# Performance work log

Measured on AMD Instinct MI355X. Metric: run time of the kernel, lower is better.

Reference implementation:

```python
import jax, jax.numpy as jnp
import numpy as np

U, D, E, L = 100000, 10000, 500000, 100000
H, O, VC = 128, 64, 20
ED = H // 4  # emb_dim = hidden // 4


def setup_inputs() -> dict:
    key = jax.random.key(0)
    it = iter(jax.random.split(key, 60))
    def nrm(shape, s=0.1):
        return jax.random.normal(next(it), shape, jnp.float32) * s
    inp = {}
    inp["x_user"] = nrm((U, 3), 1.0)
    inp["x_dest"] = nrm((D, 1), 1.0)
    inp["edge_src"] = jax.random.randint(next(it), (E,), 0, U)
    inp["edge_dst"] = jax.random.randint(next(it), (E,), 0, D)
    inp["eattr_cat"] = jax.random.randint(next(it), (E, 3), 0, VC)
    inp["eattr_num"] = nrm((E, 3), 1.0)
    inp["label_src"] = jax.random.randint(next(it), (L,), 0, U)
    inp["label_dst"] = jax.random.randint(next(it), (L,), 0, D)
    inp["user_emb"] = nrm((U, H))
    inp["dest_emb"] = nrm((D, H))
    inp["Wuf"] = nrm((3, H)); inp["buf"] = jnp.zeros((H,), jnp.float32)
    inp["Wdf"] = nrm((1, H)); inp["bdf"] = jnp.zeros((H,), jnp.float32)
    inp["emb_acc"] = nrm((VC, ED)); inp["emb_trans"] = nrm((VC, ED)); inp["emb_season"] = nrm((VC, ED))
    inp["Wnum"] = nrm((3, ED)); inp["bnum"] = jnp.zeros((ED,), jnp.float32)
    inp["Weout"] = nrm((4 * ED, H)); inp["beout"] = jnp.zeros((H,), jnp.float32)
    inp["c1v_Ws"] = nrm((H, H)); inp["c1v_Wd"] = nrm((H, H)); inp["c1v_as"] = nrm((H,)); inp["c1v_ad"] = nrm((H,))
    inp["c1v_We"] = nrm((H, H)); inp["c1v_ae"] = nrm((H,)); inp["c1v_b"] = jnp.zeros((H,), jnp.float32)
    inp["c1r_Ws"] = nrm((H, H)); inp["c1r_Wd"] = nrm((H, H)); inp["c1r_as"] = nrm((H,)); inp["c1r_ad"] = nrm((H,)); inp["c1r_b"] = jnp.zeros((H,), jnp.float32)
    inp["c2v_W"] = nrm((H, H)); inp["c2v_as"] = nrm((H,)); inp["c2v_ad"] = nrm((H,)); inp["c2v_We"] = nrm((H, H)); inp["c2v_ae"] = nrm((H,)); inp["c2v_b"] = jnp.zeros((H,), jnp.float32)
    inp["c2r_W"] = nrm((H, H)); inp["c2r_as"] = nrm((H,)); inp["c2r_ad"] = nrm((H,)); inp["c2r_b"] = jnp.zeros((H,), jnp.float32)
    inp["Wmu"] = nrm((H, O)); inp["bmu"] = jnp.zeros((O,), jnp.float32)
    inp["Wls"] = nrm((H, O)); inp["bls"] = jnp.zeros((O,), jnp.float32)
    return inp


def gat(h_src, h_dst, src, dst, Ws, Wd, a_s, a_d, bias, n_dst, ef=None, We=None, ae=None):
    """PyG GATConv, heads=1, add_self_loops=False, bipartite (src->dst)."""
    xs = h_src @ Ws  # [Ns, H]
    xd = h_dst @ Wd  # [Nd, H]
    alpha = (xs * a_s).sum(-1)[src] + (xd * a_d).sum(-1)[dst]  # [E]
    if ef is not None:
        alpha = alpha + ((ef @ We) * ae).sum(-1)
    alpha = jnp.where(alpha > 0, alpha, 0.2 * alpha)  # leaky_relu(0.2)
    amax = jax.ops.segment_max(alpha, dst, num_segments=n_dst)
    ex = jnp.exp(alpha - amax[dst])
    denom = jax.ops.segment_sum(ex, dst, num_segments=n_dst)
    w = ex / (denom[dst] + 1e-16)  # segment softmax over incoming edges
    out = jax.ops.segment_sum(w[:, None] * xs[src], dst, num_segments=n_dst)
    return out + bias


def reference(x_user, x_dest, edge_src, edge_dst, eattr_cat, eattr_num, label_src, label_dst,
              user_emb, dest_emb, Wuf, buf, Wdf, bdf,
              emb_acc, emb_trans, emb_season, Wnum, bnum, Weout, beout,
              c1v_Ws, c1v_Wd, c1v_as, c1v_ad, c1v_We, c1v_ae, c1v_b,
              c1r_Ws, c1r_Wd, c1r_as, c1r_ad, c1r_b,
              c2v_W, c2v_as, c2v_ad, c2v_We, c2v_ae, c2v_b,
              c2r_W, c2r_as, c2r_ad, c2r_b,
              Wmu, bmu, Wls, bls):
    # node encoders (full-batch: arange ids == full embedding tables)
    h_user = user_emb + x_user @ Wuf + buf  # [U, H]
    h_dest = dest_emb + x_dest @ Wdf + bdf  # [D, H]
    # EdgeBehaviorEncoder
    ef = jnp.concatenate([emb_acc[eattr_cat[:, 0]], emb_trans[eattr_cat[:, 1]],
                          emb_season[eattr_cat[:, 2]], eattr_num @ Wnum + bnum], axis=1)
    ef = ef @ Weout + beout  # [E, H]
    # layer 1
    od1 = gat(h_user, h_dest, edge_src, edge_dst, c1v_Ws, c1v_Wd, c1v_as, c1v_ad, c1v_b, D, ef, c1v_We, c1v_ae)
    ou1 = gat(h_dest, h_user, edge_dst, edge_src, c1r_Ws, c1r_Wd, c1r_as, c1r_ad, c1r_b, U)
    hu = jax.nn.relu(ou1)
    hd = jax.nn.relu(od1)
    # layer 2 (int in_channels -> shared lin for src and dst)
    od2 = gat(hu, hd, edge_src, edge_dst, c2v_W, c2v_W, c2v_as, c2v_ad, c2v_b, D, ef, c2v_We, c2v_ae)
    ou2 = gat(hd, hu, edge_dst, edge_src, c2r_W, c2r_W, c2r_as, c2r_ad, c2r_b, U)
    zu = jax.nn.relu(ou2)
    zd = jax.nn.relu(od2)
    mu_u = zu @ Wmu + bmu
    mu_d = zd @ Wmu + bmu
    ls_u = zu @ Wls + bls
    ls_d = zd @ Wls + bls
    # eval mode: reparameterize returns mu; decode = dot product on label edges
    pred = (mu_u[label_src] * mu_d[label_dst]).sum(-1)  # [L]
    return pred, mu_u, mu_d, ls_u, ls_d
```

## Files before the change

### kernel.cpp

```cpp
#include <hip/hip_runtime.h>
#include <hip/hip_bf16.h>
#include <math.h>

#define H 128
#define CDIV(a,b) (((a)+(b)-1)/(b))

__device__ __forceinline__ float wave_reduce_sum(float v){
  #pragma unroll
  for (int off = 32; off > 0; off >>= 1) v += __shfl_down(v, off, 64);
  return v;
}

__device__ __forceinline__ void wave_merge_ms(float& m, float& s){
  #pragma unroll
  for (int off = 32; off > 0; off >>= 1){
    float m2 = __shfl_xor(m, off, 64);
    float s2 = __shfl_xor(s, off, 64);
    float mn = fmaxf(m, m2);
    s = s*__expf(m - mn) + s2*__expf(m2 - mn);
    m = mn;
  }
}

__global__ __launch_bounds__(128) void k_precompute(
    const float* c1v_Wd, const float* c1v_ad,
    const float* c1r_Wd, const float* c1r_ad,
    const float* c2v_W,  const float* c2v_ad,
    const float* c2r_W,  const float* c2r_ad,
    const float* c1v_We, const float* c1v_ae,
    const float* c2v_We, const float* c2v_ae,
    const float* Weout,  const float* beout,
    const float* emb_acc, const float* emb_trans, const float* emb_season,
    const float* Wnum, const float* bnum,
    const float* Wmu, const float* Wls, const float* bmu, const float* bls,
    float* sm)
{
  const int b = blockIdx.x, t = threadIdx.x;
  if (b < 4){
    const float* M; const float* a;
    if      (b == 0){ M = c1v_Wd; a = c1v_ad; }
    else if (b == 1){ M = c1r_Wd; a = c1r_ad; }
    else if (b == 2){ M = c2v_W;  a = c2v_ad; }
    else            { M = c2r_W;  a = c2r_ad; }
    float s = 0.f;
    for (int j = 0; j < H; ++j) s += M[t*H+j] * a[j];
    sm[b*H + t] = s;
  } else if (b == 4){
    __shared__ float ws[H], vs[H];
    for (int layer = 0; layer < 2; ++layer){
      const float* We = layer ? c2v_We : c1v_We;
      const float* ae = layer ? c2v_ae : c1v_ae;
      float w = 0.f;
      for (int j = 0; j < H; ++j) w += We[t*H+j] * ae[j];
      ws[t] = w;
      __syncthreads();
      float v = 0.f;
      for (int j = 0; j < H; ++j) v += Weout[t*H+j] * ws[j];
      vs[t] = v;
      __syncthreads();
      float* tab = sm + 512 + layer*64;
      if (t < 20){
        float s1 = 0.f, s2 = 0.f, s3 = 0.f;
        for (int i = 0; i < 32; ++i){
          s1 += emb_acc   [t*32+i] * vs[i];
          s2 += emb_trans [t*32+i] * vs[32+i];
          s3 += emb_season[t*32+i] * vs[64+i];
        }
        tab[t] = s1; tab[20+t] = s2; tab[40+t] = s3;
      }
      if (t < 3){
        float s = 0.f;
        for (int i = 0; i < 32; ++i) s += Wnum[t*32+i] * vs[96+i];
        tab[60+t] = s;
      }
      if (t == 0){
        float s = 0.f;
        for (int j = 0; j < H; ++j)  s += beout[j] * ws[j];
        for (int i = 0; i < 32; ++i) s += bnum[i] * vs[96+i];
        tab[63] = s;
      }
      __syncthreads();
    }
  } else {
    float* Wcat = sm + 768;
    for (int i = (b-5)*128 + t; i < 8192; i += 7*128){
      int h = i >> 6, o = i & 63;
      Wcat[h*H + o]      = Wmu[h*64 + o];
      Wcat[h*H + 64 + o] = Wls[h*64 + o];
    }
    if (b == 5) sm[640 + t] = (t < 64) ? bmu[t] : bls[t-64];
  }
}

__global__ __launch_bounds__(256) void k_enc_user(
    const float* __restrict__ emb, const float* __restrict__ x,
    const float* __restrict__ Wf, const float* __restrict__ b,
    const float* __restrict__ qd, float* __restrict__ out,
    float* __restrict__ sout, int N)
{
  int w = (blockIdx.x*blockDim.x + threadIdx.x) >> 6;
  int lane = threadIdx.x & 63;
  if (w >= N) return;
  float2 e  = ((const float2*)emb)[(size_t)w*64 + lane];
  float x0 = x[w*3], x1 = x[w*3+1], x2 = x[w*3+2];
  float2 w0 = ((const float2*)Wf)[lane];
  float2 w1 = ((const float2*)Wf)[64+lane];
  float2 w2 = ((const float2*)Wf)[128+lane];
  float2 bb = ((const float2*)b)[lane];
  float h0 = e.x + bb.x + x0*w0.x + x1*w1.x + x2*w2.x;
  float h1 = e.y + bb.y + x0*w0.y + x1*w1.y + x2*w2.y;
  ((float2*)out)[(size_t)w*64 + lane] = make_float2(h0, h1);
  float2 q = ((const float2*)qd)[lane];
  float p = wave_reduce_sum(h0*q.x + h1*q.y);
  if (lane == 0) sout[w] = p;
}

__global__ __launch_bounds__(256) void k_enc_dest(
    const float* __restrict__ emb, const float* __restrict__ x,
    const float* __restrict__ Wf, const float* __restrict__ b,
    const float* __restrict__ qd, float* __restrict__ out,
    float* __restrict__ sout, int N)
{
  int w = (blockIdx.x*blockDim.x + threadIdx.x) >> 6;
  int lane = threadIdx.x & 63;
  if (w >= N) return;
  float2 e  = ((const float2*)emb)[(size_t)w*64 + lane];
  float x0 = x[w];
  float2 w0 = ((const float2*)Wf)[lane];
  float2 bb = ((const float2*)b)[lane];
  float h0 = e.x + bb.x + x0*w0.x;
  float h1 = e.y + bb.y + x0*w0.y;
  ((float2*)out)[(size_t)w*64 + lane] = make_float2(h0, h1);
  float2 q = ((const float2*)qd)[lane];
  float p = wave_reduce_sum(h0*q.x + h1*q.y);
  if (lane == 0) sout[w] = p;
}

__global__ __launch_bounds__(256) void k_gemm128(
    const float* __restrict__ A, const float* __restrict__ W,
    const float* __restrict__ bias, const float* __restrict__ asv,
    float* __restrict__ sout,
    float* __restrict__ out0, float* __restrict__ out1,
    int ld0, int ld1, int N)
{
  __shared__ float Ws[64][128];
  __shared__ float Xs[64][132];
  __shared__ float red[64][17];
  const int tid = threadIdx.x;
  const int rb  = blockIdx.x * 64;
  const int tc  = tid & 15, tr = tid >> 4;
  const int c0  = tc * 8;
  float C[4][8] = {};
  for (int k0 = 0; k0 < 128; k0 += 64){
    for (int i = tid; i < 2048; i += 256){
      int k = i >> 5, c4 = i & 31;
      *(float4*)&Ws[k][c4*4] = *(const float4*)&W[(size_t)(k0+k)*128 + c4*4];
    }
    for (int i = tid; i < 1024; i += 256){
      int r = i >> 4, kg = i & 15;
      int row = rb + r;
      float4 v = make_float4(0.f,0.f,0.f,0.f);
      if (row < N) v = *(const float4*)&A[(size_t)row*128 + k0 + kg*4];
      *(float4*)&Xs[r][kg*4] = v;
    }
    __syncthreads();
    #pragma unroll 4
    for (int k = 0; k < 64; ++k){
      float4 w0 = *(float4*)&Ws[k][c0];
      float4 w1 = *(float4*)&Ws[k][c0+4];
      #pragma unroll
      for (int i = 0; i < 4; ++i){
        float x = Xs[tr*4+i][k];
        C[i][0] += x*w0.x; C[i][1] += x*w0.y; C[i][2] += x*w0.z; C[i][3] += x*w0.w;
        C[i][4] += x*w1.x; C[i][5] += x*w1.y; C[i][6] += x*w1.z; C[i][7] += x*w1.w;
      }
    }
    __syncthreads();
  }
  float4 b0 = make_float4(0,0,0,0), b1 = make_float4(0,0,0,0);
  if (bias){ b0 = *(const float4*)&bias[c0]; b1 = *(const float4*)&bias[c0+4]; }
  float4 a0 = make_float4(0,0,0,0), a1 = make_float4(0,0,0,0);
  if (asv){ a0 = *(const float4*)&asv[c0]; a1 = *(const float4*)&asv[c0+4]; }
  #pragma unroll
  for (int i = 0; i < 4; ++i){
    int row = rb + tr*4 + i;
    float s = 0.f;
    if (row < N){
      float4 v0 = make_float4(C[i][0]+b0.x, C[i][1]+b0.y, C[i][2]+b0.z, C[i][3]+b0.w);
      float4 v1 = make_float4(C[i][4]+b1.x, C[i][5]+b1.y, C[i][6]+b1.z, C[i][7]+b1.w);
      if (c0 < 64){
        *(float4*)&out0[(size_t)row*ld0 + c0]     = v0;
        *(float4*)&out0[(size_t)row*ld0 + c0 + 4] = v1;
      } else {
        *(float4*)&out1[(size_t)row*ld1 + (c0-64)]     = v0;
        *(float4*)&out1[(size_t)row*ld1 + (c0-64) + 4] = v1;
      }
      if (asv){
        s = C[i][0]*a0.x + C[i][1]*a0.y + C[i][2]*a0.z + C[i][3]*a0.w
          + C[i][4]*a1.x + C[i][5]*a1.y + C[i][6]*a1.z + C[i][7]*a1.w;
      }
    }
    if (asv) red[tr*4+i][tc] = s;
  }
  if (asv){
    __syncthreads();
    if (tid < 64){
      int row = rb + tid;
      if (row < N){
        float t = 0.f;
        #pragma unroll
        for (int j = 0; j < 16; ++j) t += red[tid][j];
        sout[row] = t;
      }
    }
  }
}

__global__ void k_zero2(int* a, int na, int* b, int nb){
  int i = blockIdx.x * blockDim.x + threadIdx.x;
  if (i < na) a[i] = 0;
  else if (i - na < nb) b[i - na] = 0;
}

__global__ void k_count_both(const int* __restrict__ esrc, const int* __restrict__ edst,
                             int* __restrict__ cntU, int* __restrict__ cntD, int E){
  int e = blockIdx.x * blockDim.x + threadIdx.x;
  if (e < E){ atomicAdd(&cntU[esrc[e]], 1); atomicAdd(&cntD[edst[e]], 1); }
}

__global__ __launch_bounds__(1024) void k_scan1(const int* __restrict__ cnt,
                                                int* __restrict__ offs,
                                                int* __restrict__ bsum, int n)
{
  __shared__ int wsum[16];
  const int tid = threadIdx.x, lane = tid & 63, wid = tid >> 6;
  const int i = blockIdx.x * 1024 + tid;
  int v = (i < n) ? cnt[i] : 0;
  int inc = v;
  #pragma unroll
  for (int d = 1; d < 64; d <<= 1){
    int t2 = __shfl_up(inc, d, 64);
    if (lane >= d) inc += t2;
  }
  if (lane == 63) wsum[wid] = inc;
  __syncthreads();
  if (tid < 16){
    int x = wsum[tid];
    #pragma unroll
    for (int d = 1; d < 16; d <<= 1){
      int t2 = __shfl_up(x, d, 16);
      if (tid >= d) x += t2;
    }
    wsum[tid] = x;
  }
  __syncthreads();
  int incl = ((wid > 0) ? wsum[wid-1] : 0) + inc;
  if (i < n) offs[i+1] = incl;
  if (tid == 0) bsum[blockIdx.x] = wsum[15];
}

__global__ __launch_bounds__(1024) void k_scan2(int* __restrict__ bsum, int nb)
{
  __shared__ int wsum[16];
  const int tid = threadIdx.x, lane = tid & 63, wid = tid >> 6;
  int v = (tid < nb) ? bsum[tid] : 0;
  int inc = v;
  #pragma unroll
  for (int d = 1; d < 64; d <<= 1){
    int t2 = __shfl_up(inc, d, 64);
    if (lane >= d) inc += t2;
  }
  if (lane == 63) wsum[wid] = inc;
  __syncthreads();
  if (tid < 16){
    int x = wsum[tid];
    #pragma unroll
    for (int d = 1; d < 16; d <<= 1){
      int t2 = __shfl_up(x, d, 16);
      if (tid >= d) x += t2;
    }
    wsum[tid] = x;
  }
  __syncthreads();
  int excl = ((wid > 0) ? wsum[wid-1] : 0) + inc - v;
  if (tid < nb) bsum[tid] = excl;
}

__global__ void k_scan3(const int* __restrict__ cnt, const int* __restrict__ bsum,
                        int* __restrict__ offs, int* __restrict__ cursor, int n)
{
  int i = blockIdx.x * blockDim.x + threadIdx.x;
  if (i >= n) return;
  int v = offs[i+1] + bsum[i >> 10];
  offs[i+1] = v;
  cursor[i] = v - cnt[i];
  if (i == 0) offs[0] = 0;
}

__global__ __launch_bounds__(256) void k_scatter_both(
    const int* __restrict__ esrc, const int* __restrict__ edst,
    const int* __restrict__ ecat, const float* __restrict__ enum_,
    const float* __restrict__ tab1, const float* __restrict__ tab2,
    int* __restrict__ curU, int* __restrict__ curD,
    int4* __restrict__ recD, int* __restrict__ srtOU, int E)
{
  int e = blockIdx.x * blockDim.x + threadIdx.x;
  if (e >= E) return;
  int s = esrc[e], d = edst[e];
  int c0 = ecat[e*3], c1i = ecat[e*3+1], c2i = ecat[e*3+2];
  float n0 = enum_[e*3], n1 = enum_[e*3+1], n2 = enum_[e*3+2];
  float cA = tab1[c0] + tab1[20+c1i] + tab1[40+c2i]
           + n0*tab1[60] + n1*tab1[61] + n2*tab1[62] + tab1[63];
  float cB = tab2[c0] + tab2[20+c1i] + tab2[40+c2i]
           + n0*tab2[60] + n1*tab2[61] + n2*tab2[62] + tab2[63];
  int pD = atomicAdd(&curD[d], 1);
  recD[pD] = make_int4(s, __float_as_int(cA), __float_as_int(cB), 0);
  int pU = atomicAdd(&curU[s], 1);
  srtOU[pU] = d;
}

__global__ __launch_bounds__(256) void k_agg_v(
    const int* __restrict__ offs, const int4* __restrict__ rec,
    const float* __restrict__ gS, const float* __restrict__ selfS, int lsel,
    const float* __restrict__ xs, const float* __restrict__ bias,
    float* __restrict__ out, const float* __restrict__ qd,
    float* __restrict__ sout, int N)
{
  int w = (blockIdx.x*blockDim.x + threadIdx.x) >> 6;
  int lane = threadIdx.x & 63;
  if (w >= N) return;
  const int beg = offs[w], end = offs[w+1];
  const float uni = selfS[w];

  float m = -1e30f, s = 0.f;
  for (int base = beg; base < end; base += 64){
    int i = base + lane;
    if (i < end){
      int4 r = rec[i];
      float a = gS[r.x] + uni + __int_as_float(lsel ? r.z : r.y);
      a = a > 0.f ? a : 0.2f * a;
      float mn = fmaxf(m, a);
      s = s*__expf(m - mn) + __expf(a - mn);
      m = mn;
    }
  }
  wave_merge_ms(m, s);
  const float inv = 1.f / (s + 1e-16f);

  float a0 = 0.f, a1 = 0.f;
  const float2* xs2 = (const float2*)xs;
  for (int base = beg; base < end; base += 64){
    int i = base + lane;
    int o = 0; float wgt = 0.f;
    if (i < end){
      int4 r = rec[i];
      o = r.x;
      float a = gS[o] + uni + __int_as_float(lsel ? r.z : r.y);
      a = a > 0.f ? a : 0.2f * a;
      wgt = __expf(a - m) * inv;
    }
    int nn = min(64, end - base);
    for (int j = 0; j < nn; ++j){
      int   oo = __shfl(o, j, 64);
      float ww = __shfl(wgt, j, 64);
      float2 v = xs2[(size_t)oo*64 + lane];
      a0 += ww * v.x; a1 += ww * v.y;
    }
  }
  float2 bb = ((const float2*)bias)[lane];
  float r0 = fmaxf(a0 + bb.x, 0.f);
  float r1 = fmaxf(a1 + bb.y, 0.f);
  ((float2*)out)[(size_t)w*64 + lane] = make_float2(r0, r1);
  if (qd){
    float2 q = ((const float2*)qd)[lane];
    float p = wave_reduce_sum(r0*q.x + r1*q.y);
    if (lane == 0) sout[w] = p;
  }
}

__global__ __launch_bounds__(256) void k_agg_r(
    const int* __restrict__ offs, const int* __restrict__ srtO,
    const float* __restrict__ gS, const float* __restrict__ selfS,
    const float* __restrict__ xs, const float* __restrict__ bias,
    float* __restrict__ out, const float* __restrict__ qd,
    float* __restrict__ sout, int N)
{
  int w = (blockIdx.x*blockDim.x + threadIdx.x) >> 6;
  int lane = threadIdx.x & 63;
  if (w >= N) return;
  const int beg = offs[w], end = offs[w+1];
  const float uni = selfS[w];

  float m = -1e30f, s = 0.f;
  for (int base = beg; base < end; base += 64){
    int i = base + lane;
    if (i < end){
      float a = gS[srtO[i]] + uni;
      a = a > 0.f ? a : 0.2f * a;
      float mn = fmaxf(m, a);
      s = s*__expf(m - mn) + __expf(a - mn);
      m = mn;
    }
  }
  wave_merge_ms(m, s);
  const float inv = 1.f / (s + 1e-16f);

  float a0 = 0.f, a1 = 0.f;
  const float2* xs2 = (const float2*)xs;
  for (int base = beg; base < end; base += 64){
    int i = base + lane;
    int o = 0; float wgt = 0.f;
    if (i < end){
      o = srtO[i];
      float a = gS[o] + uni;
      a = a > 0.f ? a : 0.2f * a;
      wgt = __expf(a - m) * inv;
    }
    int nn = min(64, end - base);
    for (int j = 0; j < nn; ++j){
      int   oo = __shfl(o, j, 64);
      float ww = __shfl(wgt, j, 64);
      float2 v = xs2[(size_t)oo*64 + lane];
      a0 += ww * v.x; a1 += ww * v.y;
    }
  }
  float2 bb = ((const float2*)bias)[lane];
  float r0 = fmaxf(a0 + bb.x, 0.f);
  float r1 = fmaxf(a1 + bb.y, 0.f);
  ((float2*)out)[(size_t)w*64 + lane] = make_float2(r0, r1);
  if (qd){
    float2 q = ((const float2*)qd)[lane];
    float p = wave_reduce_sum(r0*q.x + r1*q.y);
    if (lane == 0) sout[w] = p;
  }
}

__global__ void k_pred(const int* __restrict__ ls, const int* __restrict__ ld,
                       const float* __restrict__ mu_u, const float* __restrict__ mu_d,
                       float* __restrict__ pred, int L)
{
  int wid  = (blockIdx.x * blockDim.x + threadIdx.x) >> 6;
  int lane = threadIdx.x & 63;
  if (wid >= L) return;
  float p = mu_u[(size_t)ls[wid]*64 + lane] * mu_d[(size_t)ld[wid]*64 + lane];
  p = wave_reduce_sum(p);
  if (lane == 0) pred[wid] = p;
}

extern "C" void kernel_launch(void* const* d_in, const int* in_sizes, int n_in,
                              void* d_out, int out_size, void* d_ws, size_t ws_size,
                              hipStream_t stream)
{
  (void)n_in; (void)out_size; (void)ws_size;
  const float* x_user    = (const float*)d_in[0];
  const float* x_dest    = (const float*)d_in[1];
  const int*   edge_src  = (const int*)d_in[2];
  const int*   edge_dst  = (const int*)d_in[3];
  const int*   eattr_cat = (const int*)d_in[4];
  const float* eattr_num = (const float*)d_in[5];
  const int*   label_src = (const int*)d_in[6];
  const int*   label_dst = (const int*)d_in[7];
  const float* user_emb  = (const float*)d_in[8];
  const float* dest_emb  = (const float*)d_in[9];
  const float* Wuf = (const float*)d_in[10]; const float* buf_ = (const float*)d_in[11];
  const float* Wdf = (const float*)d_in[12]; const float* bdf  = (const float*)d_in[13];
  const float* emb_acc    = (const float*)d_in[14];
  const float* emb_trans  = (const float*)d_in[15];
  const float* emb_season = (const float*)d_in[16];
  const float* Wnum = (const float*)d_in[17]; const float* bnum  = (const float*)d_in[18];
  const float* Weout = (const float*)d_in[19]; const float* beout = (const float*)d_in[20];
  const float* c1v_Ws = (const float*)d_in[21]; const float* c1v_Wd = (const float*)d_in[22];
  const float* c1v_as = (const float*)d_in[23]; const float* c1v_ad = (const float*)d_in[24];
  const float* c1v_We = (const float*)d_in[25]; const float* c1v_ae = (const float*)d_in[26];
  const float* c1v_b  = (const float*)d_in[27];
  const float* c1r_Ws = (const float*)d_in[28]; const float* c1r_Wd = (const float*)d_in[29];
  const float* c1r_as = (const float*)d_in[30]; const float* c1r_ad = (const float*)d_in[31];
  const float* c1r_b  = (const float*)d_in[32];
  const float* c2v_W  = (const float*)d_in[33]; const float* c2v_as = (const float*)d_in[34];
  const float* c2v_ad = (const float*)d_in[35]; const float* c2v_We = (const float*)d_in[36];
  const float* c2v_ae = (const float*)d_in[37]; const float* c2v_b  = (const float*)d_in[38];
  const float* c2r_W  = (const float*)d_in[39]; const float* c2r_as = (const float*)d_in[40];
  const float* c2r_ad = (const float*)d_in[41]; const float* c2r_b  = (const float*)d_in[42];
  const float* Wmu = (const float*)d_in[43]; const float* bmu = (const float*)d_in[44];
  const float* Wls = (const float*)d_in[45]; const float* bls = (const float*)d_in[46];

  const int U = in_sizes[0] / 3;
  const int D = in_sizes[1];
  const int E = in_sizes[2];
  const int L = in_sizes[6];
  const int O = 64;
  const int nbD = CDIV(D, 1024), nbU = CDIV(U, 1024);

  float* fw = (float*)d_ws;
  size_t off = 0;
  auto falloc = [&](size_t n)->float*{ float* p = fw + off; off += (n + 3) & ~(size_t)3; return p; };
  float* A    = falloc((size_t)U * H);
  float* BIG  = falloc((size_t)U * H);
  float* Bd   = falloc((size_t)D * H);
  float* SM   = falloc((size_t)D * H);
  float* sUa  = falloc(U);
  float* sUb  = falloc(U);
  float* sDa  = falloc(D);
  float* sDb  = falloc(D);
  float* sml  = falloc(17152);
  int* iw = (int*)(fw + off);
  size_t ioff = 0;
  auto ialloc = [&](size_t n)->int*{ int* p = iw + ioff; ioff += (n + 3) & ~(size_t)3; return p; };
  int* recD  = ialloc((size_t)E * 4);
  int* srtOU = ialloc(E);
  int* cntD  = ialloc(D);
  int* curD  = ialloc(D);
  int* offsD = ialloc((size_t)D + 1);
  int* cntU  = ialloc(U);
  int* curU  = ialloc(U);
  int* offsU = ialloc((size_t)U + 1);
  int* bsumD = ialloc(1024);
  int* bsumU = ialloc(1024);

  float* outp = (float*)d_out;
  float* pred = outp;
  float* mu_u = outp + L;
  float* mu_d = mu_u + (size_t)U * O;
  float* ls_u = mu_d + (size_t)D * O;
  float* ls_d = ls_u + (size_t)U * O;

  hipLaunchKernelGGL(k_precompute, dim3(12), dim3(128), 0, stream,
                     c1v_Wd, c1v_ad, c1r_Wd, c1r_ad, c2v_W, c2v_ad, c2r_W, c2r_ad,
                     c1v_We, c1v_ae, c2v_We, c2v_ae, Weout, beout,
                     emb_acc, emb_trans, emb_season, Wnum, bnum, Wmu, Wls, bmu, bls, sml);
  hipLaunchKernelGGL(k_enc_user, dim3(CDIV(U,4)), dim3(256), 0, stream,
                     user_emb, x_user, Wuf, buf_, sml+128, A, sUb, U);
  hipLaunchKernelGGL(k_enc_dest, dim3(CDIV(D,4)), dim3(256), 0, stream,
                     dest_emb, x_dest, Wdf, bdf, sml+0, Bd, sDa, D);

  hipLaunchKernelGGL(k_zero2, dim3(CDIV(U+D,256)), dim3(256), 0, stream, cntU, U, cntD, D);
  hipLaunchKernelGGL(k_count_both, dim3(CDIV(E,256)), dim3(256), 0, stream,
                     edge_src, edge_dst, cntU, cntD, E);
  hipLaunchKernelGGL(k_scan1, dim3(nbD), dim3(1024), 0, stream, cntD, offsD, bsumD, D);
  hipLaunchKernelGGL(k_scan1, dim3(nbU), dim3(1024), 0, stream, cntU, offsU, bsumU, U);
  hipLaunchKernelGGL(k_scan2, dim3(1), dim3(1024), 0, stream, bsumD, nbD);
  hipLaunchKernelGGL(k_scan2, dim3(1), dim3(1024), 0, stream, bsumU, nbU);
  hipLaunchKernelGGL(k_scan3, dim3(CDIV(D,256)), dim3(256), 0, stream, cntD, bsumD, offsD, curD, D);
  hipLaunchKernelGGL(k_scan3, dim3(CDIV(U,256)), dim3(256), 0, stream, cntU, bsumU, offsU, curU, U);
  hipLaunchKernelGGL(k_scatter_both, dim3(CDIV(E,256)), dim3(256), 0, stream,
                     edge_src, edge_dst, eattr_cat, eattr_num, sml+512, sml+576,
                     curU, curD, (int4*)recD, srtOU, E);

  hipLaunchKernelGGL(k_gemm128, dim3(CDIV(U,64)), dim3(256), 0, stream,
                     A,  c1v_Ws, (const float*)nullptr, c1v_as, sUa, BIG, BIG+64, 128, 128, U);
  hipLaunchKernelGGL(k_gemm128, dim3(CDIV(D,64)), dim3(256), 0, stream,
                     Bd, c1r_Ws, (const float*)nullptr, c1r_as, sDb, SM, SM+64, 128, 128, D);
  hipLaunchKernelGGL(k_agg_v, dim3(CDIV(D,4)), dim3(256), 0, stream,
                     offsD, (const int4*)recD, sUa, sDa, 0, BIG, c1v_b, Bd, sml+256, sDa, D);
  hipLaunchKernelGGL(k_agg_r, dim3(CDIV(U,4)), dim3(256), 0, stream,
                     offsU, srtOU, sDb, sUb, SM, c1r_b, A, sml+384, sUb, U);

  hipLaunchKernelGGL(k_gemm128, dim3(CDIV(U,64)), dim3(256), 0, stream,
                     A,  c2v_W, (const float*)nullptr, c2v_as, sUa, BIG, BIG+64, 128, 128, U);
  hipLaunchKernelGGL(k_gemm128, dim3(CDIV(D,64)), dim3(256), 0, stream,
                     Bd, c2r_W, (const float*)nullptr, c2r_as, sDb, SM, SM+64, 128, 128, D);
  hipLaunchKernelGGL(k_agg_v, dim3(CDIV(D,4)), dim3(256), 0, stream,
                     offsD, (const int4*)recD, sUa, sDa, 1, BIG, c2v_b, Bd,
                     (const float*)nullptr, (float*)nullptr, D);
  hipLaunchKernelGGL(k_agg_r, dim3(CDIV(U,4)), dim3(256), 0, stream,
                     offsU, srtOU, sDb, sUb, SM, c2r_b, A,
                     (const float*)nullptr, (float*)nullptr, U);

  hipLaunchKernelGGL(k_gemm128, dim3(CDIV(U,64)), dim3(256), 0, stream,
                     A,  sml+768, sml+640, (const float*)nullptr, (float*)nullptr, mu_u, ls_u, 64, 64, U);
  hipLaunchKernelGGL(k_gemm128, dim3(CDIV(D,64)), dim3(256), 0, stream,
                     Bd, sml+768, sml+640, (const float*)nullptr, (float*)nullptr, mu_d, ls_d, 64, 64, D);
  hipLaunchKernelGGL(k_pred, dim3(CDIV((size_t)L*64,256)), dim3(256), 0, stream,
                     label_src, label_dst, mu_u, mu_d, pred, L);
}
```

Before: 875.5 us.

## Split dest aggregation across a 4-wave block and pack edge logits as fp16

k_agg_v now gives each destination node a full 256-thread block instead of one wave. Each dest node has about 50 incoming edges, so the four waves split the softmax pass and the feature gather, then merge max/sum and the partial accumulators through shared memory. The edge record shrinks from int4 to int2 by storing the two per-edge attention constants as packed fp16 halves, which cuts scatter and gather traffic but loses precision in those logits. Index math in the gathers also switches from size_t multiplies to 32-bit shifts.

```diff
diff --git a/kernel.cpp b/kernel.cpp
--- a/kernel.cpp
+++ b/kernel.cpp
@@ -1,5 +1,6 @@
 #include <hip/hip_runtime.h>
 #include <hip/hip_bf16.h>
+#include <hip/hip_fp16.h>
 #include <math.h>
 
 #define H 128
@@ -302,7 +303,7 @@
     const int* __restrict__ ecat, const float* __restrict__ enum_,
     const float* __restrict__ tab1, const float* __restrict__ tab2,
     int* __restrict__ curU, int* __restrict__ curD,
-    int4* __restrict__ recD, int* __restrict__ srtOU, int E)
+    int2* __restrict__ recD, int* __restrict__ srtOU, int E)
 {
   int e = blockIdx.x * blockDim.x + threadIdx.x;
   if (e >= E) return;
@@ -313,68 +314,87 @@
            + n0*tab1[60] + n1*tab1[61] + n2*tab1[62] + tab1[63];
   float cB = tab2[c0] + tab2[20+c1i] + tab2[40+c2i]
            + n0*tab2[60] + n1*tab2[61] + n2*tab2[62] + tab2[63];
+  unsigned ua = __half_as_ushort(__float2half_rn(cA));
+  unsigned ub = __half_as_ushort(__float2half_rn(cB));
+  int packed = (int)((ub << 16) | ua);
   int pD = atomicAdd(&curD[d], 1);
-  recD[pD] = make_int4(s, __float_as_int(cA), __float_as_int(cB), 0);
+  recD[pD] = make_int2(s, packed);
   int pU = atomicAdd(&curU[s], 1);
   srtOU[pU] = d;
 }
 
 __global__ __launch_bounds__(256) void k_agg_v(
-    const int* __restrict__ offs, const int4* __restrict__ rec,
+    const int* __restrict__ offs, const int2* __restrict__ rec,
     const float* __restrict__ gS, const float* __restrict__ selfS, int lsel,
     const float* __restrict__ xs, const float* __restrict__ bias,
     float* __restrict__ out, const float* __restrict__ qd,
     float* __restrict__ sout, int N)
 {
-  int w = (blockIdx.x*blockDim.x + threadIdx.x) >> 6;
-  int lane = threadIdx.x & 63;
-  if (w >= N) return;
-  const int beg = offs[w], end = offs[w+1];
-  const float uni = selfS[w];
+  __shared__ float lm[4], ls_[4];
+  __shared__ float2 lacc[4][64];
+  const int node = blockIdx.x;
+  const int tid = threadIdx.x, lane = tid & 63, wv = tid >> 6;
+  const int beg = offs[node], end = offs[node+1];
+  const float uni = selfS[node];
 
   float m = -1e30f, s = 0.f;
-  for (int base = beg; base < end; base += 64){
-    int i = base + lane;
-    if (i < end){
-      int4 r = rec[i];
-      float a = gS[r.x] + uni + __int_as_float(lsel ? r.z : r.y);
-      a = a > 0.f ? a : 0.2f * a;
-      float mn = fmaxf(m, a);
-      s = s*__expf(m - mn) + __expf(a - mn);
-      m = mn;
-    }
+  for (int i = beg + tid; i < end; i += 256){
+    int2 r = rec[i];
+    unsigned pk = (unsigned)r.y;
+    float c = __half2float(__ushort_as_half((unsigned short)(lsel ? (pk >> 16) : (pk & 0xffffu))));
+    float a = gS[r.x] + uni + c;
+    a = a > 0.f ? a : 0.2f * a;
+    float mn = fmaxf(m, a);
+    s = s*__expf(m - mn) + __expf(a - mn);
+    m = mn;
   }
   wave_merge_ms(m, s);
-  const float inv = 1.f / (s + 1e-16f);
-
+  if (lane == 0){ lm[wv] = m; ls_[wv] = s; }
+  __syncthreads();
+  float M = fmaxf(fmaxf(lm[0], lm[1]), fmaxf(lm[2], lm[3]));
+  float S = ls_[0]*__expf(lm[0]-M) + ls_[1]*__expf(lm[1]-M)
+          + ls_[2]*__expf(lm[2]-M) + ls_[3]*__expf(lm[3]-M);
+  const float inv = 1.f / (S + 1e-16f);
+
+  const int tot = end - beg;
+  const int q = (tot + 3) >> 2;
+  const int wbeg = beg + wv*q;
+  const int wend = min(end, wbeg + q);
   float a0 = 0.f, a1 = 0.f;
   const float2* xs2 = (const float2*)xs;
-  for (int base = beg; base < end; base += 64){
+  for (int base = wbeg; base < wend; base += 64){
     int i = base + lane;
     int o = 0; float wgt = 0.f;
-    if (i < end){
-      int4 r = rec[i];
+    if (i < wend){
+      int2 r = rec[i];
       o = r.x;
-      float a = gS[o] + uni + __int_as_float(lsel ? r.z : r.y);
+      unsigned pk = (unsigned)r.y;
+      float c = __half2float(__ushort_as_half((unsigned short)(lsel ? (pk >> 16) : (pk & 0xffffu))));
+      float a = gS[o] + uni + c;
       a = a > 0.f ? a : 0.2f * a;
-      wgt = __expf(a - m) * inv;
-    }
-    int nn = min(64, end - base);
+      wgt = __expf(a - M) * inv;
+    }
+    int nn = min(64, wend - base);
     for (int j = 0; j < nn; ++j){
       int   oo = __shfl(o, j, 64);
       float ww = __shfl(wgt, j, 64);
-      float2 v = xs2[(size_t)oo*64 + lane];
+      float2 v = xs2[(oo << 6) + lane];
       a0 += ww * v.x; a1 += ww * v.y;
     }
   }
-  float2 bb = ((const float2*)bias)[lane];
-  float r0 = fmaxf(a0 + bb.x, 0.f);
-  float r1 = fmaxf(a1 + bb.y, 0.f);
-  ((float2*)out)[(size_t)w*64 + lane] = make_float2(r0, r1);
-  if (qd){
-    float2 q = ((const float2*)qd)[lane];
-    float p = wave_reduce_sum(r0*q.x + r1*q.y);
-    if (lane == 0) sout[w] = p;
+  lacc[wv][lane] = make_float2(a0, a1);
+  __syncthreads();
+  if (wv == 0){
+    float2 t0 = lacc[0][lane], t1 = lacc[1][lane], t2 = lacc[2][lane], t3 = lacc[3][lane];
+    float2 bb = ((const float2*)bias)[lane];
+    float r0 = fmaxf(t0.x+t1.x+t2.x+t3.x + bb.x, 0.f);
+    float r1 = fmaxf(t0.y+t1.y+t2.y+t3.y + bb.y, 0.f);
+    ((float2*)out)[(size_t)node*64 + lane] = make_float2(r0, r1);
+    if (qd){
+      float2 qv = ((const float2*)qd)[lane];
+      float p = wave_reduce_sum(r0*qv.x + r1*qv.y);
+      if (lane == 0) sout[node] = p;
+    }
   }
 }
 
@@ -392,15 +412,12 @@
   const float uni = selfS[w];
 
   float m = -1e30f, s = 0.f;
-  for (int base = beg; base < end; base += 64){
-    int i = base + lane;
-    if (i < end){
-      float a = gS[srtO[i]] + uni;
-      a = a > 0.f ? a : 0.2f * a;
-      float mn = fmaxf(m, a);
-      s = s*__expf(m - mn) + __expf(a - mn);
-      m = mn;
-    }
+  for (int i = beg + lane; i < end; i += 64){
+    float a = gS[srtO[i]] + uni;
+    a = a > 0.f ? a : 0.2f * a;
+    float mn = fmaxf(m, a);
+    s = s*__expf(m - mn) + __expf(a - mn);
+    m = mn;
   }
   wave_merge_ms(m, s);
   const float inv = 1.f / (s + 1e-16f);
@@ -420,7 +437,7 @@
     for (int j = 0; j < nn; ++j){
       int   oo = __shfl(o, j, 64);
       float ww = __shfl(wgt, j, 64);
-      float2 v = xs2[(size_t)oo*64 + lane];
+      float2 v = xs2[(oo << 6) + lane];
       a0 += ww * v.x; a1 += ww * v.y;
     }
   }
@@ -442,7 +459,7 @@
   int wid  = (blockIdx.x * blockDim.x + threadIdx.x) >> 6;
   int lane = threadIdx.x & 63;
   if (wid >= L) return;
-  float p = mu_u[(size_t)ls[wid]*64 + lane] * mu_d[(size_t)ld[wid]*64 + lane];
+  float p = mu_u[(ls[wid] << 6) + lane] * mu_d[(ld[wid] << 6) + lane];
   p = wave_reduce_sum(p);
   if (lane == 0) pred[wid] = p;
 }
@@ -506,7 +523,7 @@
   int* iw = (int*)(fw + off);
   size_t ioff = 0;
   auto ialloc = [&](size_t n)->int*{ int* p = iw + ioff; ioff += (n + 3) & ~(size_t)3; return p; };
-  int* recD  = ialloc((size_t)E * 4);
+  int* recD  = ialloc((size_t)E * 2);
   int* srtOU = ialloc(E);
   int* cntD  = ialloc(D);
   int* curD  = ialloc(D);
@@ -544,14 +561,14 @@
   hipLaunchKernelGGL(k_scan3, dim3(CDIV(U,256)), dim3(256), 0, stream, cntU, bsumU, offsU, curU, U);
   hipLaunchKernelGGL(k_scatter_both, dim3(CDIV(E,256)), dim3(256), 0, stream,
                      edge_src, edge_dst, eattr_cat, eattr_num, sml+512, sml+576,
-                     curU, curD, (int4*)recD, srtOU, E);
+                     curU, curD, (int2*)recD, srtOU, E);
 
   hipLaunchKernelGGL(k_gemm128, dim3(CDIV(U,64)), dim3(256), 0, stream,
                      A,  c1v_Ws, (const float*)nullptr, c1v_as, sUa, BIG, BIG+64, 128, 128, U);
   hipLaunchKernelGGL(k_gemm128, dim3(CDIV(D,64)), dim3(256), 0, stream,
                      Bd, c1r_Ws, (const float*)nullptr, c1r_as, sDb, SM, SM+64, 128, 128, D);
-  hipLaunchKernelGGL(k_agg_v, dim3(CDIV(D,4)), dim3(256), 0, stream,
-                     offsD, (const int4*)recD, sUa, sDa, 0, BIG, c1v_b, Bd, sml+256, sDa, D);
+  hipLaunchKernelGGL(k_agg_v, dim3(D), dim3(256), 0, stream,
+                     offsD, (const int2*)recD, sUa, sDa, 0, BIG, c1v_b, Bd, sml+256, sDa, D);
   hipLaunchKernelGGL(k_agg_r, dim3(CDIV(U,4)), dim3(256), 0, stream,
                      offsU, srtOU, sDb, sUb, SM, c1r_b, A, sml+384, sUb, U);
 
@@ -559,8 +576,8 @@
                      A,  c2v_W, (const float*)nullptr, c2v_as, sUa, BIG, BIG+64, 128, 128, U);
   hipLaunchKernelGGL(k_gemm128, dim3(CDIV(D,64)), dim3(256), 0, stream,
                      Bd, c2r_W, (const float*)nullptr, c2r_as, sDb, SM, SM+64, 128, 128, D);
-  hipLaunchKernelGGL(k_agg_v, dim3(CDIV(D,4)), dim3(256), 0, stream,
-                     offsD, (const int4*)recD, sUa, sDa, 1, BIG, c2v_b, Bd,
+  hipLaunchKernelGGL(k_agg_v, dim3(D), dim3(256), 0, stream,
+                     offsD, (const int2*)recD, sUa, sDa, 1, BIG, c2v_b, Bd,
                      (const float*)nullptr, (float*)nullptr, D);
   hipLaunchKernelGGL(k_agg_r, dim3(CDIV(U,4)), dim3(256), 0, stream,
                      offsU, srtOU, sDb, sUb, SM, c2r_b, A,
```

Measured after the change: 867.4 us. Within noise of the previous version (-0.9%).

## Pack edge attention terms as fp16, bin scatter by node range, split waves per node

Applied to the files above, without the earlier changes.

Edge attention constants are now computed in the counting pass and packed into one int as two fp16 halves, so the destination-sorted record shrinks from int4 to int2. The scatter kernel uses a fixed grid split into 8 groups, each handling only edges whose node falls in its range, to improve atomic and write locality. The aggregation kernels now split a wave across several nodes (2 per wave for destinations, 4 per wave for users) with float4 loads, which cuts idle lanes on low-degree nodes. The fp16 packing loses precision in the attention logits, and the binned scatter reads the edge list 8 times.

```diff
diff --git a/kernel.cpp b/kernel.cpp
--- a/kernel.cpp
+++ b/kernel.cpp
@@ -1,5 +1,6 @@
 #include <hip/hip_runtime.h>
 #include <hip/hip_bf16.h>
+#include <hip/hip_fp16.h>
 #include <math.h>
 
 #define H 128
@@ -11,15 +12,10 @@
   return v;
 }
 
-__device__ __forceinline__ void wave_merge_ms(float& m, float& s){
-  #pragma unroll
-  for (int off = 32; off > 0; off >>= 1){
-    float m2 = __shfl_xor(m, off, 64);
-    float s2 = __shfl_xor(s, off, 64);
-    float mn = fmaxf(m, m2);
-    s = s*__expf(m - mn) + s2*__expf(m2 - mn);
-    m = mn;
-  }
+__device__ __forceinline__ float unpack_c(int pk, int lsel){
+  unsigned u = (unsigned)pk;
+  unsigned short h = (unsigned short)(lsel ? (u >> 16) : (u & 0xffffu));
+  return __half2float(__ushort_as_half(h));
 }
 
 __global__ __launch_bounds__(128) void k_precompute(
@@ -222,10 +218,26 @@
   else if (i - na < nb) b[i - na] = 0;
 }
 
-__global__ void k_count_both(const int* __restrict__ esrc, const int* __restrict__ edst,
-                             int* __restrict__ cntU, int* __restrict__ cntD, int E){
+__global__ __launch_bounds__(256) void k_pack_count(
+    const int* __restrict__ esrc, const int* __restrict__ edst,
+    const int* __restrict__ ecat, const float* __restrict__ enum_,
+    const float* __restrict__ tab1, const float* __restrict__ tab2,
+    int* __restrict__ cntU, int* __restrict__ cntD,
+    int* __restrict__ packed, int E)
+{
   int e = blockIdx.x * blockDim.x + threadIdx.x;
-  if (e < E){ atomicAdd(&cntU[esrc[e]], 1); atomicAdd(&cntD[edst[e]], 1); }
+  if (e >= E) return;
+  int c0 = ecat[e*3], c1i = ecat[e*3+1], c2i = ecat[e*3+2];
+  float n0 = enum_[e*3], n1 = enum_[e*3+1], n2 = enum_[e*3+2];
+  float cA = tab1[c0] + tab1[20+c1i] + tab1[40+c2i]
+           + n0*tab1[60] + n1*tab1[61] + n2*tab1[62] + tab1[63];
+  float cB = tab2[c0] + tab2[20+c1i] + tab2[40+c2i]
+           + n0*tab2[60] + n1*tab2[61] + n2*tab2[62] + tab2[63];
+  unsigned ua = __half_as_ushort(__float2half_rn(cA));
+  unsigned ub = __half_as_ushort(__float2half_rn(cB));
+  packed[e] = (int)((ub << 16) | ua);
+  atomicAdd(&cntU[esrc[e]], 1);
+  atomicAdd(&cntD[edst[e]], 1);
 }
 
 __global__ __launch_bounds__(1024) void k_scan1(const int* __restrict__ cnt,
@@ -297,84 +309,96 @@
   if (i == 0) offs[0] = 0;
 }
 
-__global__ __launch_bounds__(256) void k_scatter_both(
+__global__ __launch_bounds__(256) void k_scatter_binned(
     const int* __restrict__ esrc, const int* __restrict__ edst,
-    const int* __restrict__ ecat, const float* __restrict__ enum_,
-    const float* __restrict__ tab1, const float* __restrict__ tab2,
+    const int* __restrict__ packed,
     int* __restrict__ curU, int* __restrict__ curD,
-    int4* __restrict__ recD, int* __restrict__ srtOU, int E)
-{
-  int e = blockIdx.x * blockDim.x + threadIdx.x;
-  if (e >= E) return;
-  int s = esrc[e], d = edst[e];
-  int c0 = ecat[e*3], c1i = ecat[e*3+1], c2i = ecat[e*3+2];
-  float n0 = enum_[e*3], n1 = enum_[e*3+1], n2 = enum_[e*3+2];
-  float cA = tab1[c0] + tab1[20+c1i] + tab1[40+c2i]
-           + n0*tab1[60] + n1*tab1[61] + n2*tab1[62] + tab1[63];
-  float cB = tab2[c0] + tab2[20+c1i] + tab2[40+c2i]
-           + n0*tab2[60] + n1*tab2[61] + n2*tab2[62] + tab2[63];
-  int pD = atomicAdd(&curD[d], 1);
-  recD[pD] = make_int4(s, __float_as_int(cA), __float_as_int(cB), 0);
-  int pU = atomicAdd(&curU[s], 1);
-  srtOU[pU] = d;
+    int2* __restrict__ recD, int* __restrict__ srtOU, int E, int U, int D)
+{
+  const int grp = blockIdx.x & 7;
+  const int lb  = blockIdx.x >> 3;
+  const int GB  = gridDim.x >> 3;
+  const int D8 = CDIV(D, 8), U8 = CDIV(U, 8);
+  const int dlo = grp * D8, dhi = min(D, dlo + D8);
+  const int slo = grp * U8, shi = min(U, slo + U8);
+  for (int e = lb*256 + threadIdx.x; e < E; e += GB*256){
+    int s = esrc[e], d = edst[e];
+    if (d >= dlo && d < dhi){
+      int p = atomicAdd(&curD[d], 1);
+      recD[p] = make_int2(s, packed[e]);
+    }
+    if (s >= slo && s < shi){
+      int p = atomicAdd(&curU[s], 1);
+      srtOU[p] = d;
+    }
+  }
 }
 
 __global__ __launch_bounds__(256) void k_agg_v(
-    const int* __restrict__ offs, const int4* __restrict__ rec,
+    const int* __restrict__ offs, const int2* __restrict__ rec,
     const float* __restrict__ gS, const float* __restrict__ selfS, int lsel,
     const float* __restrict__ xs, const float* __restrict__ bias,
     float* __restrict__ out, const float* __restrict__ qd,
     float* __restrict__ sout, int N)
 {
-  int w = (blockIdx.x*blockDim.x + threadIdx.x) >> 6;
-  int lane = threadIdx.x & 63;
-  if (w >= N) return;
-  const int beg = offs[w], end = offs[w+1];
-  const float uni = selfS[w];
+  const int wid = (blockIdx.x*blockDim.x + threadIdx.x) >> 6;
+  const int lane = threadIdx.x & 63;
+  const int gl = lane & 31;
+  const int node = wid*2 + (lane >> 5);
+  if (node >= N) return;
+  const int beg = offs[node], end = offs[node+1];
+  const float uni = selfS[node];
 
   float m = -1e30f, s = 0.f;
-  for (int base = beg; base < end; base += 64){
-    int i = base + lane;
-    if (i < end){
-      int4 r = rec[i];
-      float a = gS[r.x] + uni + __int_as_float(lsel ? r.z : r.y);
-      a = a > 0.f ? a : 0.2f * a;
-      float mn = fmaxf(m, a);
-      s = s*__expf(m - mn) + __expf(a - mn);
-      m = mn;
-    }
-  }
-  wave_merge_ms(m, s);
+  for (int i = beg + gl; i < end; i += 32){
+    int2 r = rec[i];
+    float a = gS[r.x] + uni + unpack_c(r.y, lsel);
+    a = a > 0.f ? a : 0.2f * a;
+    float mn = fmaxf(m, a);
+    s = s*__expf(m - mn) + __expf(a - mn);
+    m = mn;
+  }
+  #pragma unroll
+  for (int off = 16; off > 0; off >>= 1){
+    float m2 = __shfl_xor(m, off, 64);
+    float s2 = __shfl_xor(s, off, 64);
+    float mn = fmaxf(m, m2);
+    s = s*__expf(m - mn) + s2*__expf(m2 - mn);
+    m = mn;
+  }
   const float inv = 1.f / (s + 1e-16f);
 
-  float a0 = 0.f, a1 = 0.f;
-  const float2* xs2 = (const float2*)xs;
-  for (int base = beg; base < end; base += 64){
-    int i = base + lane;
+  float4 acc = make_float4(0.f,0.f,0.f,0.f);
+  const float4* xs4 = (const float4*)xs;
+  const int gbase = lane & 32;
+  for (int base = beg; base < end; base += 32){
+    int i = base + gl;
     int o = 0; float wgt = 0.f;
     if (i < end){
-      int4 r = rec[i];
+      int2 r = rec[i];
       o = r.x;
-      float a = gS[o] + uni + __int_as_float(lsel ? r.z : r.y);
+      float a = gS[o] + uni + unpack_c(r.y, lsel);
       a = a > 0.f ? a : 0.2f * a;
       wgt = __expf(a - m) * inv;
     }
-    int nn = min(64, end - base);
+    int nn = min(32, end - base);
     for (int j = 0; j < nn; ++j){
-      int   oo = __shfl(o, j, 64);
-      float ww = __shfl(wgt, j, 64);
-      float2 v = xs2[(size_t)oo*64 + lane];
-      a0 += ww * v.x; a1 += ww * v.y;
-    }
-  }
-  float2 bb = ((const float2*)bias)[lane];
-  float r0 = fmaxf(a0 + bb.x, 0.f);
-  float r1 = fmaxf(a1 + bb.y, 0.f);
-  ((float2*)out)[(size_t)w*64 + lane] = make_float2(r0, r1);
+      int   oo = __shfl(o,   gbase + j, 64);
+      float ww = __shfl(wgt, gbase + j, 64);
+      float4 v = xs4[(oo << 5) + gl];
+      acc.x += ww*v.x; acc.y += ww*v.y; acc.z += ww*v.z; acc.w += ww*v.w;
+    }
+  }
+  float4 bb = ((const float4*)bias)[gl];
+  float4 r4 = make_float4(fmaxf(acc.x+bb.x,0.f), fmaxf(acc.y+bb.y,0.f),
+                          fmaxf(acc.z+bb.z,0.f), fmaxf(acc.w+bb.w,0.f));
+  ((float4*)out)[(node << 5) + gl] = r4;
   if (qd){
-    float2 q = ((const float2*)qd)[lane];
-    float p = wave_reduce_sum(r0*q.x + r1*q.y);
-    if (lane == 0) sout[w] = p;
+    float4 q4 = ((const float4*)qd)[gl];
+    float p = r4.x*q4.x + r4.y*q4.y + r4.z*q4.z + r4.w*q4.w;
+    #pragma unroll
+    for (int off = 16; off > 0; off >>= 1) p += __shfl_xor(p, off, 64);
+    if (gl == 0) sout[node] = p;
   }
 }
 
@@ -385,30 +409,38 @@
     float* __restrict__ out, const float* __restrict__ qd,
     float* __restrict__ sout, int N)
 {
-  int w = (blockIdx.x*blockDim.x + threadIdx.x) >> 6;
-  int lane = threadIdx.x & 63;
-  if (w >= N) return;
-  const int beg = offs[w], end = offs[w+1];
-  const float uni = selfS[w];
+  const int wid = (blockIdx.x*blockDim.x + threadIdx.x) >> 6;
+  const int lane = threadIdx.x & 63;
+  const int gl = lane & 15;
+  const int node = wid*4 + (lane >> 4);
+  if (node >= N) return;
+  const int beg = offs[node], end = offs[node+1];
+  const float uni = selfS[node];
 
   float m = -1e30f, s = 0.f;
-  for (int base = beg; base < end; base += 64){
-    int i = base + lane;
-    if (i < end){
-      float a = gS[srtO[i]] + uni;
-      a = a > 0.f ? a : 0.2f * a;
-      float mn = fmaxf(m, a);
-      s = s*__expf(m - mn) + __expf(a - mn);
-      m = mn;
-    }
-  }
-  wave_merge_ms(m, s);
+  for (int i = beg + gl; i < end; i += 16){
+    float a = gS[srtO[i]] + uni;
+    a = a > 0.f ? a : 0.2f * a;
+    float mn = fmaxf(m, a);
+    s = s*__expf(m - mn) + __expf(a - mn);
+    m = mn;
+  }
+  #pragma unroll
+  for (int off = 8; off > 0; off >>= 1){
+    float m2 = __shfl_xor(m, off, 64);
+    float s2 = __shfl_xor(s, off, 64);
+    float mn = fmaxf(m, m2);
+    s = s*__expf(m - mn) + s2*__expf(m2 - mn);
+    m = mn;
+  }
   const float inv = 1.f / (s + 1e-16f);
 
-  float a0 = 0.f, a1 = 0.f;
-  const float2* xs2 = (const float2*)xs;
-  for (int base = beg; base < end; base += 64){
-    int i = base + lane;
+  float4 acc0 = make_float4(0.f,0.f,0.f,0.f);
+  float4 acc1 = make_float4(0.f,0.f,0.f,0.f);
+  const float4* xs4 = (const float4*)xs;
+  const int gbase = lane & 48;
+  for (int base = beg; base < end; base += 16){
+    int i = base + gl;
     int o = 0; float wgt = 0.f;
     if (i < end){
       o = srtO[i];
@@ -416,22 +448,32 @@
       a = a > 0.f ? a : 0.2f * a;
       wgt = __expf(a - m) * inv;
     }
-    int nn = min(64, end - base);
+    int nn = min(16, end - base);
     for (int j = 0; j < nn; ++j){
-      int   oo = __shfl(o, j, 64);
-      float ww = __shfl(wgt, j, 64);
-      float2 v = xs2[(size_t)oo*64 + lane];
-      a0 += ww * v.x; a1 += ww * v.y;
-    }
-  }
-  float2 bb = ((const float2*)bias)[lane];
-  float r0 = fmaxf(a0 + bb.x, 0.f);
-  float r1 = fmaxf(a1 + bb.y, 0.f);
-  ((float2*)out)[(size_t)w*64 + lane] = make_float2(r0, r1);
+      int   oo = __shfl(o,   gbase + j, 64);
+      float ww = __shfl(wgt, gbase + j, 64);
+      float4 v0 = xs4[(oo << 5) + gl];
+      float4 v1 = xs4[(oo << 5) + 16 + gl];
+      acc0.x += ww*v0.x; acc0.y += ww*v0.y; acc0.z += ww*v0.z; acc0.w += ww*v0.w;
+      acc1.x += ww*v1.x; acc1.y += ww*v1.y; acc1.z += ww*v1.z; acc1.w += ww*v1.w;
+    }
+  }
+  float4 b0 = ((const float4*)bias)[gl];
+  float4 b1 = ((const float4*)bias)[16 + gl];
+  float4 r0 = make_float4(fmaxf(acc0.x+b0.x,0.f), fmaxf(acc0.y+b0.y,0.f),
+                          fmaxf(acc0.z+b0.z,0.f), fmaxf(acc0.w+b0.w,0.f));
+  float4 r1 = make_float4(fmaxf(acc1.x+b1.x,0.f), fmaxf(acc1.y+b1.y,0.f),
+                          fmaxf(acc1.z+b1.z,0.f), fmaxf(acc1.w+b1.w,0.f));
+  ((float4*)out)[(node << 5) + gl]      = r0;
+  ((float4*)out)[(node << 5) + 16 + gl] = r1;
   if (qd){
-    float2 q = ((const float2*)qd)[lane];
-    float p = wave_reduce_sum(r0*q.x + r1*q.y);
-    if (lane == 0) sout[w] = p;
+    float4 q0 = ((const float4*)qd)[gl];
+    float4 q1 = ((const float4*)qd)[16 + gl];
+    float p = r0.x*q0.x + r0.y*q0.y + r0.z*q0.z + r0.w*q0.w
+            + r1.x*q1.x + r1.y*q1.y + r1.z*q1.z + r1.w*q1.w;
+    #pragma unroll
+    for (int off = 8; off > 0; off >>= 1) p += __shfl_xor(p, off, 64);
+    if (gl == 0) sout[node] = p;
   }
 }
 
@@ -442,7 +484,7 @@
   int wid  = (blockIdx.x * blockDim.x + threadIdx.x) >> 6;
   int lane = threadIdx.x & 63;
   if (wid >= L) return;
-  float p = mu_u[(size_t)ls[wid]*64 + lane] * mu_d[(size_t)ld[wid]*64 + lane];
+  float p = mu_u[(ls[wid] << 6) + lane] * mu_d[(ld[wid] << 6) + lane];
   p = wave_reduce_sum(p);
   if (lane == 0) pred[wid] = p;
 }
@@ -506,8 +548,9 @@
   int* iw = (int*)(fw + off);
   size_t ioff = 0;
   auto ialloc = [&](size_t n)->int*{ int* p = iw + ioff; ioff += (n + 3) & ~(size_t)3; return p; };
-  int* recD  = ialloc((size_t)E * 4);
+  int* recD  = ialloc((size_t)E * 2);
   int* srtOU = ialloc(E);
+  int* packed= ialloc(E);
   int* cntD  = ialloc(D);
   int* curD  = ialloc(D);
   int* offsD = ialloc((size_t)D + 1);
@@ -534,35 +577,35 @@
                      dest_emb, x_dest, Wdf, bdf, sml+0, Bd, sDa, D);
 
   hipLaunchKernelGGL(k_zero2, dim3(CDIV(U+D,256)), dim3(256), 0, stream, cntU, U, cntD, D);
-  hipLaunchKernelGGL(k_count_both, dim3(CDIV(E,256)), dim3(256), 0, stream,
-                     edge_src, edge_dst, cntU, cntD, E);
+  hipLaunchKernelGGL(k_pack_count, dim3(CDIV(E,256)), dim3(256), 0, stream,
+                     edge_src, edge_dst, eattr_cat, eattr_num, sml+512, sml+576,
+                     cntU, cntD, packed, E);
   hipLaunchKernelGGL(k_scan1, dim3(nbD), dim3(1024), 0, stream, cntD, offsD, bsumD, D);
   hipLaunchKernelGGL(k_scan1, dim3(nbU), dim3(1024), 0, stream, cntU, offsU, bsumU, U);
   hipLaunchKernelGGL(k_scan2, dim3(1), dim3(1024), 0, stream, bsumD, nbD);
   hipLaunchKernelGGL(k_scan2, dim3(1), dim3(1024), 0, stream, bsumU, nbU);
   hipLaunchKernelGGL(k_scan3, dim3(CDIV(D,256)), dim3(256), 0, stream, cntD, bsumD, offsD, curD, D);
   hipLaunchKernelGGL(k_scan3, dim3(CDIV(U,256)), dim3(256), 0, stream, cntU, bsumU, offsU, curU, U);
-  hipLaunchKernelGGL(k_scatter_both, dim3(CDIV(E,256)), dim3(256), 0, stream,
-                     edge_src, edge_dst, eattr_cat, eattr_num, sml+512, sml+576,
-                     curU, curD, (int4*)recD, srtOU, E);
+  hipLaunchKernelGGL(k_scatter_binned, dim3(512), dim3(256), 0, stream,
+                     edge_src, edge_dst, packed, curU, curD, (int2*)recD, srtOU, E, U, D);
 
   hipLaunchKernelGGL(k_gemm128, dim3(CDIV(U,64)), dim3(256), 0, stream,
                      A,  c1v_Ws, (const float*)nullptr, c1v_as, sUa, BIG, BIG+64, 128, 128, U);
   hipLaunchKernelGGL(k_gemm128, dim3(CDIV(D,64)), dim3(256), 0, stream,
                      Bd, c1r_Ws, (const float*)nullptr, c1r_as, sDb, SM, SM+64, 128, 128, D);
-  hipLaunchKernelGGL(k_agg_v, dim3(CDIV(D,4)), dim3(256), 0, stream,
-                     offsD, (const int4*)recD, sUa, sDa, 0, BIG, c1v_b, Bd, sml+256, sDa, D);
-  hipLaunchKernelGGL(k_agg_r, dim3(CDIV(U,4)), dim3(256), 0, stream,
+  hipLaunchKernelGGL(k_agg_v, dim3(CDIV(D,8)), dim3(256), 0, stream,
+                     offsD, (const int2*)recD, sUa, sDa, 0, BIG, c1v_b, Bd, sml+256, sDa, D);
+  hipLaunchKernelGGL(k_agg_r, dim3(CDIV(U,16)), dim3(256), 0, stream,
                      offsU, srtOU, sDb, sUb, SM, c1r_b, A, sml+384, sUb, U);
 
   hipLaunchKernelGGL(k_gemm128, dim3(CDIV(U,64)), dim3(256), 0, stream,
                      A,  c2v_W, (const float*)nullptr, c2v_as, sUa, BIG, BIG+64, 128, 128, U);
   hipLaunchKernelGGL(k_gemm128, dim3(CDIV(D,64)), dim3(256), 0, stream,
                      Bd, c2r_W, (const float*)nullptr, c2r_as, sDb, SM, SM+64, 128, 128, D);
-  hipLaunchKernelGGL(k_agg_v, dim3(CDIV(D,4)), dim3(256), 0, stream,
-                     offsD, (const int4*)recD, sUa, sDa, 1, BIG, c2v_b, Bd,
+  hipLaunchKernelGGL(k_agg_v, dim3(CDIV(D,8)), dim3(256), 0, stream,
+                     offsD, (const int2*)recD, sUa, sDa, 1, BIG, c2v_b, Bd,
                      (const float*)nullptr, (float*)nullptr, D);
-  hipLaunchKernelGGL(k_agg_r, dim3(CDIV(U,4)), dim3(256), 0, stream,
+  hipLaunchKernelGGL(k_agg_r, dim3(CDIV(U,16)), dim3(256), 0, stream,
                      offsU, srtOU, sDb, sUb, SM, c2r_b, A,
                      (const float*)nullptr, (float*)nullptr, U);
 
```

New measurement: 792.4 us. -9.5%, faster.
